# Performance work log

Measured on AMD Instinct MI355X. Metric: run time of the kernel, lower is better.

## Reference

```python
import jax, jax.numpy as jnp
import numpy as np

H = 12          # num heads
D = 768         # hidden size
DH = D // H     # size per head
FF = 3072       # intermediate size
EPS = 1e-11


def gelu(x):
    # tanh approximation, matching the TF source exactly
    c = np.sqrt(2.0 / np.pi).astype(np.float32)
    return x * 0.5 * (1.0 + jnp.tanh(c * (x + 0.044715 * jnp.power(x, 3))))


def layer_norm(x, gamma, beta):
    mean = jnp.mean(x, axis=-1, keepdims=True)
    var = jnp.mean(jnp.square(x - mean), axis=-1, keepdims=True)
    return (x - mean) * jax.lax.rsqrt(var + EPS) * gamma + beta


def setup_inputs() -> dict:
    key = jax.random.key(0)
    ks = jax.random.split(key, 12)
    B, S = 16, 512
    std = 0.02
    inp = {
        "x": jax.random.normal(ks[0], (B, S, D), jnp.float32),
        "mask": jnp.ones((B, S), dtype=bool),
        "Wq": jax.random.normal(ks[1], (D, D), jnp.float32) * std,
        "bq": jnp.zeros((D,), jnp.float32),
        "Wk": jax.random.normal(ks[2], (D, D), jnp.float32) * std,
        "bk": jnp.zeros((D,), jnp.float32),
        "Wv": jax.random.normal(ks[3], (D, D), jnp.float32) * std,
        "bv": jnp.zeros((D,), jnp.float32),
        "Wo": jax.random.normal(ks[4], (D, D), jnp.float32) * std,
        "bo": jnp.zeros((D,), jnp.float32),
        "g1": jnp.ones((D,), jnp.float32),
        "b1": jnp.zeros((D,), jnp.float32),
        "Wi": jax.random.normal(ks[5], (D, FF), jnp.float32) * std,
        "bi": jnp.zeros((FF,), jnp.float32),
        "Wo2": jax.random.normal(ks[6], (FF, D), jnp.float32) * std,
        "bo2": jnp.zeros((D,), jnp.float32),
        "g2": jnp.ones((D,), jnp.float32),
        "b2": jnp.zeros((D,), jnp.float32),
    }
    return inp


def reference(x, mask, Wq, bq, Wk, bk, Wv, bv, Wo, bo, g1, b1, Wi, bi, Wo2, bo2, g2, b2):
    B, S, _ = x.shape
    # QKV projections
    q = (x @ Wq + bq).reshape(B, S, H, DH)
    k = (x @ Wk + bk).reshape(B, S, H, DH)
    v = (x @ Wv + bv).reshape(B, S, H, DH)
    # scaled dot-product attention scores [B, H, S, S]
    scores = jnp.einsum("bqhd,bkhd->bhqk", q, k) / np.sqrt(DH).astype(np.float32)
    # key-side mask, applied as score * m + (1 - m) * -100 (per original source)
    m = mask[:, None, None, :].astype(jnp.float32)
    scores = scores * m + (1.0 - m) * (-100.0)
    probs = jax.nn.softmax(scores, axis=-1)
    attn = jnp.einsum("bhqk,bkhd->bqhd", probs, v).reshape(B, S, D)
    # tf.boolean_mask with all-True mask -> flatten batch and seq dims
    attn = attn.reshape(B * S, D)
    x_flat = x.reshape(B * S, D)
    # attention output projection + residual + LN
    attn_out = layer_norm(attn @ Wo + bo + x_flat, g1, b1)
    # FFN: gelu dense then output dense + residual + LN
    inter = gelu(attn_out @ Wi + bi)
    out = layer_norm(inter @ Wo2 + bo2 + attn_out, g2, b2)
    return out
```

## Files before the change

### kernel.cpp

```cpp
#include <hip/hip_runtime.h>


#define DEV __device__ __forceinline__

typedef unsigned short u16;
typedef unsigned int   u32;
typedef __bf16 bf16x8 __attribute__((ext_vector_type(8)));
typedef float  f32x4  __attribute__((ext_vector_type(4)));
typedef unsigned short u16x8 __attribute__((ext_vector_type(8)));
typedef unsigned short u16x4 __attribute__((ext_vector_type(4)));

DEV u16 f2bf(float f) {
    u32 u = __builtin_bit_cast(u32, f);
    u += 0x7fffu + ((u >> 16) & 1u);
    return (u16)(u >> 16);
}
DEV float bf2f(u16 u) { u32 x = (u32)u << 16; return __builtin_bit_cast(float, x); }

DEV float gelu_f(float x) {
    float u = 0.7978845608028654f * (x + 0.044715f * x * x * x);
    float e = __expf(2.f * u);
    return 0.5f * x * (2.f - 2.f / (e + 1.f));
}

DEV void gload16(const void* gsrc, void* ldst) {
    __builtin_amdgcn_global_load_lds(
        (__attribute__((address_space(1))) void*)(void*)(const_cast<void*>(gsrc)),
        (__attribute__((address_space(3))) void*)ldst, 16, 0, 0);
}

DEV f32x4 MFMA(bf16x8 a, bf16x8 b, f32x4 c) {
    return __builtin_amdgcn_mfma_f32_16x16x32_bf16(a, b, c, 0, 0, 0);
}

__global__ __launch_bounds__(256) void prep(
    const float* __restrict__ x, const float* __restrict__ Wq,
    const float* __restrict__ Wk, const float* __restrict__ Wv,
    const float* __restrict__ Wo, const float* __restrict__ Wi,
    const float* __restrict__ Wo2, const float* __restrict__ bq,
    const float* __restrict__ bk, const float* __restrict__ bv,
    u16* __restrict__ Xb, u16* __restrict__ WqkvT, u16* __restrict__ WoT,
    u16* __restrict__ WiT, u16* __restrict__ Wo2T, float* __restrict__ bqkv) {
    __shared__ float tile[32][33];
    int bid = blockIdx.x, t = threadIdx.x;
    if (bid < 6144) {
        int i = (bid * 256 + t) * 4;
        f32x4 v = *(const f32x4*)(x + i);
        u16x4 o;
        o.x = f2bf(v.x); o.y = f2bf(v.y); o.z = f2bf(v.z); o.w = f2bf(v.w);
        *(u16x4*)(Xb + i) = o;
        return;
    }
    bid -= 6144;
    if (bid >= 6912) {
        int i = (bid - 6912) * 256 + t;
        if (i < 2304)
            bqkv[i] = (i < 768) ? bq[i] : (i < 1536 ? bk[i - 768] : bv[i - 1536]);
        return;
    }
    const float* in; u16* out; int R, C, bx, by;
    if (bid < 1728) {
        int w = bid / 576, idx = bid % 576;
        in = (w == 0) ? Wq : (w == 1) ? Wk : Wv;
        out = WqkvT + (size_t)w * 768 * 768;
        R = 768; C = 768; bx = idx % 24; by = idx / 24;
    } else if (bid < 2304) {
        int idx = bid - 1728;
        in = Wo; out = WoT; R = 768; C = 768; bx = idx % 24; by = idx / 24;
    } else if (bid < 4608) {
        int idx = bid - 2304;
        in = Wi; out = WiT; R = 768; C = 3072; bx = idx % 96; by = idx / 96;
    } else {
        int idx = bid - 4608;
        in = Wo2; out = Wo2T; R = 3072; C = 768; bx = idx % 24; by = idx / 24;
    }
    int tx = t & 31, ty = t >> 5;
    int r0 = by * 32, c0 = bx * 32;
#pragma unroll
    for (int i = 0; i < 4; i++)
        tile[ty + i * 8][tx] = in[(size_t)(r0 + ty + i * 8) * C + c0 + tx];
    __syncthreads();
#pragma unroll
    for (int i = 0; i < 4; i++)
        out[(size_t)(c0 + ty + i * 8) * R + r0 + tx] = f2bf(tile[tx][ty + i * 8]);
}

template <int EPI>
DEV void gemm_g4_body(const u16* __restrict__ A, const u16* __restrict__ BT,
                      const float* __restrict__ bias, void* __restrict__ Cout,
                      int N, int K, int ntn) {
    __shared__ __align__(16) char smem[73728];
    const int t = threadIdx.x, lane = t & 63, wid = t >> 6;
    const int nwg = gridDim.x, bid = blockIdx.x;
    const int swzb = ((nwg & 7) == 0) ? ((bid & 7) * (nwg >> 3) + (bid >> 3)) : bid;
    const int tm = swzb / ntn, tn = swzb % ntn;
    const int wm = wid >> 1, wn = wid & 1;

    f32x4 acc[4][4];
#pragma unroll
    for (int i = 0; i < 4; i++)
#pragma unroll
        for (int j = 0; j < 4; j++) acc[i][j] = f32x4{0.f, 0.f, 0.f, 0.f};

    const int NT = K >> 5;
    const u16* Ab = A + (size_t)tm * 256 * K;
    const u16* Bb = BT + (size_t)tn * 128 * K;

    int ra[2], ca[2];
#pragma unroll
    for (int j = 0; j < 2; j++) {
        int X = t * 16 + j * 8192;
        int Y = X ^ (((X >> 7) & 7) << 4);
        ra[j] = Y >> 6; ca[j] = (Y & 63) >> 1;
    }
    const u16* pA0 = Ab + (size_t)ra[0] * K + ca[0];
    const u16* pA1 = Ab + (size_t)ra[1] * K + ca[1];
    const u16* pB0 = Bb + (size_t)ra[0] * K + ca[0];
    const int dA0 = t * 16, dA1 = t * 16 + 8192, dB = 16384 + t * 16;

    const int g16 = (lane >> 4) << 4;
    const int rA = wm * 64 + (lane & 15);
    const int rB = wn * 64 + (lane & 15);
    const int aoff = (rA * 64 + g16) ^ (((rA >> 1) & 7) << 4);
    const int boff = 16384 + ((rB * 64 + g16) ^ (((rB >> 1) & 7) << 4));

#define STG4(TT)                                                      \
    {                                                                 \
        char* s_ = smem + ((TT) % 3) * 24576;                         \
        int ko_ = (TT) * 32;                                          \
        gload16(pA0 + ko_, s_ + dA0);                                 \
        gload16(pA1 + ko_, s_ + dA1);                                 \
        gload16(pB0 + ko_, s_ + dB);                                  \
    }

    STG4(0) STG4(1)
    asm volatile("s_waitcnt vmcnt(3)" ::: "memory");
    __builtin_amdgcn_s_barrier();
    asm volatile("" ::: "memory");

    for (int tt = 0; tt < NT; ++tt) {
        if (tt + 2 < NT) STG4(tt + 2)
        const char* buf = smem + (tt % 3) * 24576;
        bf16x8 af[4], bfr[4];
#pragma unroll
        for (int mi = 0; mi < 4; mi++) af[mi] = *(const bf16x8*)(buf + aoff + mi * 1024);
#pragma unroll
        for (int ni = 0; ni < 4; ni++) bfr[ni] = *(const bf16x8*)(buf + boff + ni * 1024);
        __builtin_amdgcn_s_setprio(1);
#pragma unroll
        for (int mi = 0; mi < 4; mi++)
#pragma unroll
            for (int ni = 0; ni < 4; ni++)
                acc[mi][ni] = MFMA(af[mi], bfr[ni], acc[mi][ni]);
        __builtin_amdgcn_s_setprio(0);
        if (tt + 1 < NT) {
            if (tt + 2 < NT) asm volatile("s_waitcnt vmcnt(3)" ::: "memory");
            else             asm volatile("s_waitcnt vmcnt(0)" ::: "memory");
        }
        __builtin_amdgcn_s_barrier();
        asm volatile("" ::: "memory");
    }
#undef STG4

    const int r0 = tm * 256 + wm * 64, c0 = tn * 128 + wn * 64;
    float bcol[4];
#pragma unroll
    for (int ni = 0; ni < 4; ni++) bcol[ni] = bias[c0 + ni * 16 + (lane & 15)];
#pragma unroll
    for (int mi = 0; mi < 4; mi++) {
#pragma unroll
        for (int r = 0; r < 4; r++) {
            int gr = r0 + mi * 16 + ((lane >> 4) << 2) + r;
#pragma unroll
            for (int ni = 0; ni < 4; ni++) {
                int gc = c0 + ni * 16 + (lane & 15);
                float v = acc[mi][ni][r] + bcol[ni];
                if constexpr (EPI == 2) v = gelu_f(v);
                ((u16*)Cout)[(size_t)gr * N + gc] = f2bf(v);
            }
        }
    }
}

__global__ __launch_bounds__(512, 2) void g4_qkv(const u16* A, const u16* BT,
                                                 const float* bias, void* C,
                                                 int N, int K, int ntn) {
    gemm_g4_body<0>(A, BT, bias, C, N, K, ntn);
}
__global__ __launch_bounds__(512, 2) void g4_ffn1(const u16* A, const u16* BT,
                                                  const float* bias, void* C,
                                                  int N, int K, int ntn) {
    gemm_g4_body<2>(A, BT, bias, C, N, K, ntn);
}

template <int EPI>
DEV void gemm_c3_body(const u16* __restrict__ A, const u16* __restrict__ BT,
                      const float* __restrict__ bias, const void* __restrict__ res,
                      void* __restrict__ Cout, int N, int K, int ntn) {
    __shared__ __align__(16) char smem[49152];
    const int t = threadIdx.x, lane = t & 63, wid = t >> 6;
    const int nwg = gridDim.x, bid = blockIdx.x;
    const int swzb = ((nwg & 7) == 0) ? ((bid & 7) * (nwg >> 3) + (bid >> 3)) : bid;
    const int tm = swzb / ntn, tn = swzb % ntn;
    const int wm = wid >> 1, wn = wid & 1;

    f32x4 acc[4][4];
#pragma unroll
    for (int i = 0; i < 4; i++)
#pragma unroll
        for (int j = 0; j < 4; j++) acc[i][j] = f32x4{0.f, 0.f, 0.f, 0.f};

    const int NT = K >> 5;
    const u16* Ab = A + (size_t)tm * 128 * K;
    const u16* Bb = BT + (size_t)tn * 128 * K;

    int sr[2], sc[2];
#pragma unroll
    for (int j = 0; j < 2; j++) {
        int X = t * 16 + j * 4096;
        int Y = X ^ (((X >> 7) & 7) << 4);
        sr[j] = Y >> 6; sc[j] = (Y & 63) >> 1;
    }
    const u16* pA0 = Ab + (size_t)sr[0] * K + sc[0];
    const u16* pA1 = Ab + (size_t)sr[1] * K + sc[1];
    const u16* pB0 = Bb + (size_t)sr[0] * K + sc[0];
    const u16* pB1 = Bb + (size_t)sr[1] * K + sc[1];
    const int d0 = wid * 1024, d1 = wid * 1024 + 4096;

    const int g16 = (lane >> 4) << 4;
    const int rA = wm * 64 + (lane & 15);
    const int rB = wn * 64 + (lane & 15);
    const int aoff = (rA * 64 + g16) ^ (((rA >> 1) & 7) << 4);
    const int boff = 8192 + ((rB * 64 + g16) ^ (((rB >> 1) & 7) << 4));

#define STG(TT)                                                       \
    {                                                                 \
        char* s_ = smem + ((TT) % 3) * 16384;                         \
        int ko_ = (TT) * 32;                                          \
        gload16(pA0 + ko_, s_ + d0);                                  \
        gload16(pA1 + ko_, s_ + d1);                                  \
        gload16(pB0 + ko_, s_ + 8192 + d0);                           \
        gload16(pB1 + ko_, s_ + 8192 + d1);                           \
    }

    STG(0) STG(1)
    asm volatile("s_waitcnt vmcnt(4)" ::: "memory");
    __builtin_amdgcn_s_barrier();
    asm volatile("" ::: "memory");

    for (int tt = 0; tt < NT; ++tt) {
        if (tt + 2 < NT) STG(tt + 2)
        const char* buf = smem + (tt % 3) * 16384;
        bf16x8 af[4], bfr[4];
#pragma unroll
        for (int mi = 0; mi < 4; mi++) af[mi] = *(const bf16x8*)(buf + aoff + mi * 1024);
#pragma unroll
        for (int ni = 0; ni < 4; ni++) bfr[ni] = *(const bf16x8*)(buf + boff + ni * 1024);
        __builtin_amdgcn_s_setprio(1);
#pragma unroll
        for (int mi = 0; mi < 4; mi++)
#pragma unroll
            for (int ni = 0; ni < 4; ni++)
                acc[mi][ni] = MFMA(af[mi], bfr[ni], acc[mi][ni]);
        __builtin_amdgcn_s_setprio(0);
        if (tt + 1 < NT) {
            if (tt + 2 < NT) asm volatile("s_waitcnt vmcnt(4)" ::: "memory");
            else             asm volatile("s_waitcnt vmcnt(0)" ::: "memory");
        }
        __builtin_amdgcn_s_barrier();
        asm volatile("" ::: "memory");
    }
#undef STG

    const int r0 = tm * 128 + wm * 64, c0 = tn * 128 + wn * 64;
    float bcol[4];
#pragma unroll
    for (int ni = 0; ni < 4; ni++) bcol[ni] = bias[c0 + ni * 16 + (lane & 15)];
#pragma unroll
    for (int mi = 0; mi < 4; mi++) {
#pragma unroll
        for (int r = 0; r < 4; r++) {
            int gr = r0 + mi * 16 + ((lane >> 4) << 2) + r;
#pragma unroll
            for (int ni = 0; ni < 4; ni++) {
                int gc = c0 + ni * 16 + (lane & 15);
                float v = acc[mi][ni][r] + bcol[ni];
                if constexpr (EPI == 3)
                    v += ((const float*)res)[(size_t)gr * N + gc];
                if constexpr (EPI == 4)
                    v += bf2f(((const u16*)res)[(size_t)gr * N + gc]);
                ((u16*)Cout)[(size_t)gr * N + gc] = f2bf(v);
            }
        }
    }
}

__global__ __launch_bounds__(256, 3) void g3_wo(const u16* A, const u16* BT,
                                                const float* bias, const void* res,
                                                void* C, int N, int K, int ntn) {
    gemm_c3_body<3>(A, BT, bias, res, C, N, K, ntn);
}
__global__ __launch_bounds__(256, 3) void g3_ffn2(const u16* A, const u16* BT,
                                                  const float* bias, const void* res,
                                                  void* C, int N, int K, int ntn) {
    gemm_c3_body<4>(A, BT, bias, res, C, N, K, ntn);
}

__global__ __launch_bounds__(256) void attn_kernel(const u16* __restrict__ QKV,
                                                   u16* __restrict__ attnb) {
    __shared__ __align__(16) char sm[24576];
    char* Ks = sm;
    char* Vt = sm + 8192;
    const int t = threadIdx.x, lane = t & 63, wid = t >> 6;
    const int qt = blockIdx.x, bh = blockIdx.y;
    const int b = bh / 12, h = bh % 12;
    const size_t base = (size_t)b * 512 * 2304;
    char* Pw = sm + 16384 + wid * 2048;

    bf16x8 aq[2];
    {
        int qrow = qt * 64 + wid * 16 + (lane & 15);
        const u16* qp = QKV + base + (size_t)qrow * 2304 + h * 64 + ((lane >> 4) << 3);
        aq[0] = *(const bf16x8*)qp;
        aq[1] = *(const bf16x8*)(qp + 32);
    }
    f32x4 oacc[4];
#pragma unroll
    for (int g = 0; g < 4; g++) oacc[g] = f32x4{0.f, 0.f, 0.f, 0.f};
    float mrun[4] = {-1e30f, -1e30f, -1e30f, -1e30f};
    float lrun[4] = {0.f, 0.f, 0.f, 0.f};

    for (int kt = 0; kt < 8; ++kt) {
        __syncthreads();
#pragma unroll
        for (int i = 0; i < 2; i++) {
            int cw = wid * 2 + i;
            int o = cw * 1024 + lane * 16;
            int row = o >> 7;
            int cb = (o & 127) ^ ((row & 7) << 4);
            gload16(QKV + base + (size_t)(kt * 64 + row) * 2304 + 768 + h * 64 + (cb >> 1),
                    Ks + cw * 1024);
        }
        {
            int key = t & 63, dh0 = wid * 16;
            const u16* vp = QKV + base + (size_t)(kt * 64 + key) * 2304 + 1536 + h * 64 + dh0;
            u16x8 v0 = *(const u16x8*)vp;
            u16x8 v1 = *(const u16x8*)(vp + 8);
#pragma unroll
            for (int j = 0; j < 8; j++) {
                int dh = dh0 + j;
                *(u16*)(Vt + dh * 128 + ((key * 2) ^ ((dh & 7) << 4))) = v0[j];
            }
#pragma unroll
            for (int j = 0; j < 8; j++) {
                int dh = dh0 + 8 + j;
                *(u16*)(Vt + dh * 128 + ((key * 2) ^ ((dh & 7) << 4))) = v1[j];
            }
        }
        __syncthreads();

        f32x4 sacc[4];
#pragma unroll
        for (int ni = 0; ni < 4; ni++) sacc[ni] = f32x4{0.f, 0.f, 0.f, 0.f};
#pragma unroll
        for (int ni = 0; ni < 4; ni++) {
            int row = ni * 16 + (lane & 15);
#pragma unroll
            for (int ks = 0; ks < 2; ks++) {
                int cb = (ks * 64 + ((lane >> 4) << 4)) ^ ((row & 7) << 4);
                bf16x8 bk = *(const bf16x8*)(Ks + row * 128 + cb);
                sacc[ni] = MFMA(aq[ks], bk, sacc[ni]);
            }
        }
#pragma unroll
        for (int ni = 0; ni < 4; ni++)
#pragma unroll
            for (int r = 0; r < 4; r++) sacc[ni][r] *= 0.125f;

#pragma unroll
        for (int r = 0; r < 4; r++) {
            float pm = fmaxf(fmaxf(sacc[0][r], sacc[1][r]), fmaxf(sacc[2][r], sacc[3][r]));
            pm = fmaxf(pm, __shfl_xor(pm, 1));
            pm = fmaxf(pm, __shfl_xor(pm, 2));
            pm = fmaxf(pm, __shfl_xor(pm, 4));
            pm = fmaxf(pm, __shfl_xor(pm, 8));
            float mnew = fmaxf(mrun[r], pm);
            float sf = __expf(mrun[r] - mnew);
            mrun[r] = mnew;
            lrun[r] *= sf;
#pragma unroll
            for (int g = 0; g < 4; g++) oacc[g][r] *= sf;
            int prow = ((lane >> 4) << 2) + r;
            float ps = 0.f;
#pragma unroll
            for (int ni = 0; ni < 4; ni++) {
                float p = __expf(sacc[ni][r] - mnew);
                ps += p;
                int col = ni * 16 + (lane & 15);
                *(u16*)(Pw + prow * 128 + ((col * 2) ^ ((prow & 7) << 4))) = f2bf(p);
            }
            ps += __shfl_xor(ps, 1);
            ps += __shfl_xor(ps, 2);
            ps += __shfl_xor(ps, 4);
            ps += __shfl_xor(ps, 8);
            lrun[r] += ps;
        }
        __syncthreads();

#pragma unroll
        for (int ks = 0; ks < 2; ks++) {
            int prow = lane & 15;
            int pcb = (ks * 64 + ((lane >> 4) << 4)) ^ ((prow & 7) << 4);
            bf16x8 ap = *(const bf16x8*)(Pw + prow * 128 + pcb);
#pragma unroll
            for (int g = 0; g < 4; g++) {
                int vrow = g * 16 + (lane & 15);
                int vcb = (ks * 64 + ((lane >> 4) << 4)) ^ ((vrow & 7) << 4);
                bf16x8 bv = *(const bf16x8*)(Vt + vrow * 128 + vcb);
                oacc[g] = MFMA(ap, bv, oacc[g]);
            }
        }
    }

#pragma unroll
    for (int g = 0; g < 4; g++)
#pragma unroll
        for (int r = 0; r < 4; r++) {
            int qrow = qt * 64 + wid * 16 + ((lane >> 4) << 2) + r;
            float o = oacc[g][r] / lrun[r];
            attnb[(size_t)(b * 512 + qrow) * 768 + h * 64 + g * 16 + (lane & 15)] = f2bf(o);
        }
}

template <int OUTF>
__global__ __launch_bounds__(256) void ln_s(const u16* __restrict__ S,
                                            const float* __restrict__ g,
                                            const float* __restrict__ bta,
                                            void* __restrict__ out) {
    int row = blockIdx.x, t = threadIdx.x, lane = t & 63, wid = t >> 6;
    const u16* s = S + (size_t)row * 768;
    float v[3];
#pragma unroll
    for (int i = 0; i < 3; i++) v[i] = bf2f(s[t + i * 256]);

    float sum = v[0] + v[1] + v[2];
#pragma unroll
    for (int o = 32; o; o >>= 1) sum += __shfl_xor(sum, o);
    __shared__ float sm[4];
    __shared__ float bc[2];
    if (lane == 0) sm[wid] = sum;
    __syncthreads();
    if (t == 0) bc[0] = (sm[0] + sm[1] + sm[2] + sm[3]) * (1.f / 768.f);
    __syncthreads();
    float mean = bc[0];

    float q = 0.f;
#pragma unroll
    for (int i = 0; i < 3; i++) { float d = v[i] - mean; q += d * d; }
#pragma unroll
    for (int o = 32; o; o >>= 1) q += __shfl_xor(q, o);
    if (lane == 0) sm[wid] = q;
    __syncthreads();
    if (t == 0) bc[1] = rsqrtf((sm[0] + sm[1] + sm[2] + sm[3]) * (1.f / 768.f) + 1e-11f);
    __syncthreads();
    float rs = bc[1];
#pragma unroll
    for (int i = 0; i < 3; i++) {
        int c = t + i * 256;
        float o = (v[i] - mean) * rs * g[c] + bta[c];
        if constexpr (OUTF)
            ((float*)out)[(size_t)row * 768 + c] = o;
        else
            ((u16*)out)[(size_t)row * 768 + c] = f2bf(o);
    }
}

extern "C" void kernel_launch(void* const* d_in, const int* in_sizes, int n_in,
                              void* d_out, int out_size, void* d_ws, size_t ws_size,
                              hipStream_t stream) {
    const float* x   = (const float*)d_in[0];
    const float* Wq  = (const float*)d_in[2];
    const float* bq  = (const float*)d_in[3];
    const float* Wk  = (const float*)d_in[4];
    const float* bk  = (const float*)d_in[5];
    const float* Wv  = (const float*)d_in[6];
    const float* bv  = (const float*)d_in[7];
    const float* Wo  = (const float*)d_in[8];
    const float* bo  = (const float*)d_in[9];
    const float* g1  = (const float*)d_in[10];
    const float* b1  = (const float*)d_in[11];
    const float* Wi  = (const float*)d_in[12];
    const float* bi  = (const float*)d_in[13];
    const float* Wo2 = (const float*)d_in[14];
    const float* bo2 = (const float*)d_in[15];
    const float* g2  = (const float*)d_in[16];
    const float* b2  = (const float*)d_in[17];

    char* w = (char*)d_ws;
    size_t off = 0;
    auto alloc = [&](size_t n) { size_t o = off; off += (n + 255) & ~(size_t)255; return o; };
    size_t oXb    = alloc((size_t)8192 * 768 * 2);
    size_t oWqkvT = alloc((size_t)2304 * 768 * 2);
    size_t oWoT   = alloc((size_t)768 * 768 * 2);
    size_t oWiT   = alloc((size_t)3072 * 768 * 2);
    size_t oWo2T  = alloc((size_t)768 * 3072 * 2);
    size_t oBqkv  = alloc((size_t)2304 * 4);
    size_t oR0    = alloc((size_t)8192 * 3072 * 2);
    size_t oYb    = alloc((size_t)8192 * 768 * 2);
    size_t oAob   = alloc((size_t)8192 * 768 * 2);
    (void)ws_size; (void)in_sizes; (void)n_in; (void)out_size;

    u16*   Xb    = (u16*)(w + oXb);
    u16*   WqkvT = (u16*)(w + oWqkvT);
    u16*   WoT   = (u16*)(w + oWoT);
    u16*   WiT   = (u16*)(w + oWiT);
    u16*   Wo2T  = (u16*)(w + oWo2T);
    float* bqkv  = (float*)(w + oBqkv);
    u16*   QKV   = (u16*)(w + oR0);
    u16*   attnb = (u16*)(w + oR0 + (size_t)8192 * 2304 * 2);
    u16*   inter = (u16*)(w + oR0);
    u16*   Yb    = (u16*)(w + oYb);
    u16*   aob   = (u16*)(w + oAob);

    prep<<<13065, 256, 0, stream>>>(x, Wq, Wk, Wv, Wo, Wi, Wo2, bq, bk, bv,
                                    Xb, WqkvT, WoT, WiT, Wo2T, bqkv);
    g4_qkv<<<576, 512, 0, stream>>>(Xb, WqkvT, bqkv, QKV, 2304, 768, 18);
    attn_kernel<<<dim3(8, 192), 256, 0, stream>>>(QKV, attnb);
    g3_wo<<<384, 256, 0, stream>>>(attnb, WoT, bo, x, Yb, 768, 768, 6);
    ln_s<0><<<8192, 256, 0, stream>>>(Yb, g1, b1, aob);
    g4_ffn1<<<768, 512, 0, stream>>>(aob, WiT, bi, inter, 3072, 768, 24);
    g3_ffn2<<<384, 256, 0, stream>>>(inter, Wo2T, bo2, aob, Yb, 768, 3072, 6);
    ln_s<1><<<8192, 256, 0, stream>>>(Yb, g2, b2, (float*)d_out);
}
```

Before: 258.6 us.

## Halve GEMM workgroup to 4 waves with 128x64 per-wave tiles

The QKV and FFN1 GEMMs now run 256-thread workgroups (4 waves) instead of 512, and each wave computes a 128x64 sub-tile with 8x4 MFMA accumulators instead of 64x64. The 256x128 block tile stays the same, so each thread issues six 16-byte global-to-LDS loads per K step. The aim is more MFMA work per LDS fragment load and less barrier overhead per wave. The cost is doubled accumulator registers, which may limit occupancy, and fewer waves available to hide latency.

Result: no change. 259.7 us (+0.4%).

```diff
diff --git a/kernel.cpp b/kernel.cpp
--- a/kernel.cpp
+++ b/kernel.cpp
@@ -86,7 +86,7 @@
 }
 
 template <int EPI>
-DEV void gemm_g4_body(const u16* __restrict__ A, const u16* __restrict__ BT,
+DEV void gemm_g5_body(const u16* __restrict__ A, const u16* __restrict__ BT,
                       const float* __restrict__ bias, void* __restrict__ Cout,
                       int N, int K, int ntn) {
     __shared__ __align__(16) char smem[73728];
@@ -96,84 +96,91 @@
     const int tm = swzb / ntn, tn = swzb % ntn;
     const int wm = wid >> 1, wn = wid & 1;
 
-    f32x4 acc[4][4];
-#pragma unroll
-    for (int i = 0; i < 4; i++)
-#pragma unroll
-        for (int j = 0; j < 4; j++) acc[i][j] = f32x4{0.f, 0.f, 0.f, 0.f};
+    f32x4 acc[8][4];
+#pragma unroll
+    for (int m = 0; m < 8; m++)
+#pragma unroll
+        for (int n = 0; n < 4; n++) acc[m][n] = f32x4{0.f, 0.f, 0.f, 0.f};
 
     const int NT = K >> 5;
     const u16* Ab = A + (size_t)tm * 256 * K;
     const u16* Bb = BT + (size_t)tn * 128 * K;
 
-    int ra[2], ca[2];
-#pragma unroll
-    for (int j = 0; j < 2; j++) {
-        int X = t * 16 + j * 8192;
+    int ar[4], ac[4];
+#pragma unroll
+    for (int j = 0; j < 4; j++) {
+        int X = t * 16 + j * 4096;
         int Y = X ^ (((X >> 7) & 7) << 4);
-        ra[j] = Y >> 6; ca[j] = (Y & 63) >> 1;
-    }
-    const u16* pA0 = Ab + (size_t)ra[0] * K + ca[0];
-    const u16* pA1 = Ab + (size_t)ra[1] * K + ca[1];
-    const u16* pB0 = Bb + (size_t)ra[0] * K + ca[0];
-    const int dA0 = t * 16, dA1 = t * 16 + 8192, dB = 16384 + t * 16;
-
-    const int g16 = (lane >> 4) << 4;
-    const int rA = wm * 64 + (lane & 15);
-    const int rB = wn * 64 + (lane & 15);
-    const int aoff = (rA * 64 + g16) ^ (((rA >> 1) & 7) << 4);
-    const int boff = 16384 + ((rB * 64 + g16) ^ (((rB >> 1) & 7) << 4));
-
-#define STG4(TT)                                                      \
+        ar[j] = Y >> 6; ac[j] = (Y & 63) >> 1;
+    }
+    const u16* pA0 = Ab + (size_t)ar[0] * K + ac[0];
+    const u16* pA1 = Ab + (size_t)ar[1] * K + ac[1];
+    const u16* pA2 = Ab + (size_t)ar[2] * K + ac[2];
+    const u16* pA3 = Ab + (size_t)ar[3] * K + ac[3];
+    const u16* pB0 = Bb + (size_t)ar[0] * K + ac[0];
+    const u16* pB1 = Bb + (size_t)ar[1] * K + ac[1];
+    const int dT = t * 16;
+
+    const int l15 = lane & 15, g16 = (lane >> 4) << 4;
+    const int key = (l15 >> 1) << 4;
+    const int rA = wm * 128 + l15;
+    const int rB = wn * 64 + l15;
+    const int aoff = (rA * 64 + g16) ^ key;
+    const int boff = 16384 + ((rB * 64 + g16) ^ key);
+
+#define STG5(TT)                                                      \
     {                                                                 \
         char* s_ = smem + ((TT) % 3) * 24576;                         \
         int ko_ = (TT) * 32;                                          \
-        gload16(pA0 + ko_, s_ + dA0);                                 \
-        gload16(pA1 + ko_, s_ + dA1);                                 \
-        gload16(pB0 + ko_, s_ + dB);                                  \
-    }
-
-    STG4(0) STG4(1)
-    asm volatile("s_waitcnt vmcnt(3)" ::: "memory");
+        gload16(pA0 + ko_, s_ + dT);                                  \
+        gload16(pA1 + ko_, s_ + 4096 + dT);                           \
+        gload16(pA2 + ko_, s_ + 8192 + dT);                           \
+        gload16(pA3 + ko_, s_ + 12288 + dT);                          \
+        gload16(pB0 + ko_, s_ + 16384 + dT);                          \
+        gload16(pB1 + ko_, s_ + 20480 + dT);                          \
+    }
+
+    STG5(0) STG5(1)
+    asm volatile("s_waitcnt vmcnt(6)" ::: "memory");
     __builtin_amdgcn_s_barrier();
     asm volatile("" ::: "memory");
 
     for (int tt = 0; tt < NT; ++tt) {
-        if (tt + 2 < NT) STG4(tt + 2)
+        if (tt + 2 < NT) STG5(tt + 2)
         const char* buf = smem + (tt % 3) * 24576;
-        bf16x8 af[4], bfr[4];
-#pragma unroll
-        for (int mi = 0; mi < 4; mi++) af[mi] = *(const bf16x8*)(buf + aoff + mi * 1024);
+        bf16x8 af[8], bfr[4];
 #pragma unroll
         for (int ni = 0; ni < 4; ni++) bfr[ni] = *(const bf16x8*)(buf + boff + ni * 1024);
+#pragma unroll
+        for (int mi = 0; mi < 8; mi++) af[mi] = *(const bf16x8*)(buf + aoff + mi * 1024);
         __builtin_amdgcn_s_setprio(1);
 #pragma unroll
-        for (int mi = 0; mi < 4; mi++)
+        for (int mi = 0; mi < 8; mi++)
 #pragma unroll
             for (int ni = 0; ni < 4; ni++)
                 acc[mi][ni] = MFMA(af[mi], bfr[ni], acc[mi][ni]);
         __builtin_amdgcn_s_setprio(0);
         if (tt + 1 < NT) {
-            if (tt + 2 < NT) asm volatile("s_waitcnt vmcnt(3)" ::: "memory");
+            if (tt + 2 < NT) asm volatile("s_waitcnt vmcnt(6)" ::: "memory");
             else             asm volatile("s_waitcnt vmcnt(0)" ::: "memory");
         }
         __builtin_amdgcn_s_barrier();
         asm volatile("" ::: "memory");
     }
-#undef STG4
-
-    const int r0 = tm * 256 + wm * 64, c0 = tn * 128 + wn * 64;
+#undef STG5
+
+    const int r0 = tm * 256 + wm * 128, c0 = tn * 128 + wn * 64;
     float bcol[4];
 #pragma unroll
-    for (int ni = 0; ni < 4; ni++) bcol[ni] = bias[c0 + ni * 16 + (lane & 15)];
-#pragma unroll
-    for (int mi = 0; mi < 4; mi++) {
+    for (int ni = 0; ni < 4; ni++) bcol[ni] = bias[c0 + ni * 16 + l15];
+#pragma unroll
+    for (int mi = 0; mi < 8; mi++) {
 #pragma unroll
         for (int r = 0; r < 4; r++) {
             int gr = r0 + mi * 16 + ((lane >> 4) << 2) + r;
 #pragma unroll
             for (int ni = 0; ni < 4; ni++) {
-                int gc = c0 + ni * 16 + (lane & 15);
+                int gc = c0 + ni * 16 + l15;
                 float v = acc[mi][ni][r] + bcol[ni];
                 if constexpr (EPI == 2) v = gelu_f(v);
                 ((u16*)Cout)[(size_t)gr * N + gc] = f2bf(v);
@@ -182,15 +189,15 @@
     }
 }
 
-__global__ __launch_bounds__(512, 2) void g4_qkv(const u16* A, const u16* BT,
+__global__ __launch_bounds__(256, 2) void g5_qkv(const u16* A, const u16* BT,
                                                  const float* bias, void* C,
                                                  int N, int K, int ntn) {
-    gemm_g4_body<0>(A, BT, bias, C, N, K, ntn);
-}
-__global__ __launch_bounds__(512, 2) void g4_ffn1(const u16* A, const u16* BT,
+    gemm_g5_body<0>(A, BT, bias, C, N, K, ntn);
+}
+__global__ __launch_bounds__(256, 2) void g5_ffn1(const u16* A, const u16* BT,
                                                   const float* bias, void* C,
                                                   int N, int K, int ntn) {
-    gemm_g4_body<2>(A, BT, bias, C, N, K, ntn);
+    gemm_g5_body<2>(A, BT, bias, C, N, K, ntn);
 }
 
 template <int EPI>
@@ -524,11 +531,11 @@
 
     prep<<<13065, 256, 0, stream>>>(x, Wq, Wk, Wv, Wo, Wi, Wo2, bq, bk, bv,
                                     Xb, WqkvT, WoT, WiT, Wo2T, bqkv);
-    g4_qkv<<<576, 512, 0, stream>>>(Xb, WqkvT, bqkv, QKV, 2304, 768, 18);
+    g5_qkv<<<576, 256, 0, stream>>>(Xb, WqkvT, bqkv, QKV, 2304, 768, 18);
     attn_kernel<<<dim3(8, 192), 256, 0, stream>>>(QKV, attnb);
     g3_wo<<<384, 256, 0, stream>>>(attnb, WoT, bo, x, Yb, 768, 768, 6);
     ln_s<0><<<8192, 256, 0, stream>>>(Yb, g1, b1, aob);
-    g4_ffn1<<<768, 512, 0, stream>>>(aob, WiT, bi, inter, 3072, 768, 24);
+    g5_ffn1<<<768, 256, 0, stream>>>(aob, WiT, bi, inter, 3072, 768, 24);
     g3_ffn2<<<384, 256, 0, stream>>>(inter, Wo2T, bo2, aob, Yb, 768, 3072, 6);
     ln_s<1><<<8192, 256, 0, stream>>>(Yb, g2, b2, (float*)d_out);
 }
```
